# Performance work log

Measured on AMD Instinct MI355X. Metric: run time of the kernel, lower is better.

The kernel has to match this reference:

```python
import jax, jax.numpy as jnp
import numpy as np
from jax import lax


def _batch_conv(x, w, b):
    # x: [B, Cin, H, W], w: [B, Cout, Cin, kh, kw], b: [B, Cout]
    # Per-sample conv (the torch code's groups=B grouped-conv trick),
    # expressed as vmap over the batch of an ordinary conv.
    def one(xi, wi):
        return lax.conv_general_dilated(
            xi[None], wi, window_strides=(1, 1), padding='SAME',
            dimension_numbers=('NCHW', 'OIHW', 'NCHW'))[0]
    y = jax.vmap(one)(x, w)                       # [B, Cout, H, W]
    return y + b[:, :, None, None]


def setup_inputs() -> dict:
    key = jax.random.key(0)
    ks = jax.random.split(key, 9)
    B, Cin, H, W = 32, 3, 64, 64
    NC = 10
    s = 0.05
    return {
        'x': jax.random.normal(ks[0], (B, Cin, H, W), jnp.float32),
        'conv1_weight': jax.random.normal(ks[1], (B, 64, Cin, 3, 3), jnp.float32) * s,
        'conv2_weight': jax.random.normal(ks[2], (B, 128, 64, 3, 3), jnp.float32) * s,
        'conv3_weight': jax.random.normal(ks[3], (B, 256, 128, 3, 3), jnp.float32) * s,
        'fc_weight': jax.random.normal(ks[4], (B, 1, NC), jnp.float32) * s,
        'bias1': jax.random.normal(ks[5], (B, 64), jnp.float32) * s,
        'bias2': jax.random.normal(ks[6], (B, 128), jnp.float32) * s,
        'bias3': jax.random.normal(ks[7], (B, 256), jnp.float32) * s,
        'bias4': jax.random.normal(ks[8], (B, NC), jnp.float32) * s,
    }


def reference(x, conv1_weight, conv2_weight, conv3_weight, fc_weight,
              bias1, bias2, bias3, bias4):
    h = jax.nn.relu(_batch_conv(x, conv1_weight, bias1))   # [B, 64, H, W]
    h = jax.nn.relu(_batch_conv(h, conv2_weight, bias2))   # [B, 128, H, W]
    h = jax.nn.relu(_batch_conv(h, conv3_weight, bias3))   # [B, 256, H, W]
    h = jnp.mean(h, axis=(2, 3))                           # AdaptiveAvgPool2d(1) -> [B, 256]
    h = h[:, :, None]                                      # view(B, N, -1) -> [B, 256, 1]
    # BatchLinearLayer: bmm(x, weight) + bias
    out = jnp.einsum('bnd,bdo->bno', h, fc_weight) + bias4[:, None, :]  # [B, 256, 10]
    return out
```

## Files before the change

kernel.cpp:

```cpp
#include <hip/hip_runtime.h>
#include <stdint.h>

typedef __attribute__((ext_vector_type(8))) short short8;
typedef __attribute__((ext_vector_type(16))) float f32x16;

#define NB 32

__device__ __forceinline__ float bf2f(uint16_t v) {
    return __uint_as_float(((uint32_t)v) << 16);
}
__device__ __forceinline__ uint16_t f2bf(float f) {
    uint32_t u = __float_as_uint(f);
    u += 0x7fffu + ((u >> 16) & 1u);
    return (uint16_t)(u >> 16);
}

__device__ __forceinline__ void gload16(const void* g, void* l) {
    __builtin_amdgcn_global_load_lds(
        (const __attribute__((address_space(1))) uint32_t*)g,
        (__attribute__((address_space(3))) uint32_t*)l, 16, 0, 0);
}

template<int COUT, int CIN>
__device__ __forceinline__ void prep_w_item(int idx, const float* __restrict__ w,
                                            uint16_t* __restrict__ wp)
{
    const int ci = idx % CIN;
    const int t  = idx / CIN;
    const int oc = t % COUT;
    const int b  = t / COUT;
    const float* s = w + (size_t)idx * 9;
    #pragma unroll
    for (int k = 0; k < 9; k++)
        wp[((size_t)(b * 9 + k) * COUT + oc) * CIN + ci] = f2bf(s[k]);
}

__global__ __launch_bounds__(256) void prep_w3_k(
    const float* __restrict__ w, uint16_t* __restrict__ wp)
{
    const int idx = blockIdx.x * 256 + threadIdx.x;
    if (idx < NB * 256 * 128) prep_w_item<256, 128>(idx, w, wp);
}

template<bool DO_W3>
__global__ __launch_bounds__(256) void prep_all(
    const float* __restrict__ x,  const float* __restrict__ w1,
    const float* __restrict__ w2, const float* __restrict__ w3,
    uint16_t* __restrict__ xp,  uint16_t* __restrict__ wp1,
    uint16_t* __restrict__ wp2, uint16_t* __restrict__ wp3,
    float* __restrict__ zp)
{
    int idx = blockIdx.x * 256 + threadIdx.x;
    if (idx < 4096) {
        ((float4*)zp)[idx] = make_float4(0.f, 0.f, 0.f, 0.f);
        return;
    }
    idx -= 4096;
    if (idx < 131072) {
        const int xc = idx & 63, y = (idx >> 6) & 63, b = idx >> 12;
        const float* s = x + (size_t)b * 3 * 4096 + y * 64 + xc;
        const uint16_t v0 = f2bf(s[0]), v1 = f2bf(s[4096]), v2 = f2bf(s[8192]);
        short8 lo = {(short)v0, (short)v1, (short)v2, 0, 0, 0, 0, 0};
        short8 hi = {0, 0, 0, 0, 0, 0, 0, 0};
        uint16_t* d = xp + (size_t)idx * 16;
        *(short8*)d = lo;
        *(short8*)(d + 8) = hi;
        return;
    }
    idx -= 131072;
    if (idx < 18432) {
        const int oc = idx & 63, k = (idx >> 6) % 9, b = idx / 576;
        const uint16_t v0 = f2bf(w1[((size_t)(b * 64 + oc) * 3 + 0) * 9 + k]);
        const uint16_t v1 = f2bf(w1[((size_t)(b * 64 + oc) * 3 + 1) * 9 + k]);
        const uint16_t v2 = f2bf(w1[((size_t)(b * 64 + oc) * 3 + 2) * 9 + k]);
        short8 lo = {(short)v0, (short)v1, (short)v2, 0, 0, 0, 0, 0};
        short8 hi = {0, 0, 0, 0, 0, 0, 0, 0};
        uint16_t* d = wp1 + ((size_t)(b * 9 + k) * 64 + oc) * 16;
        *(short8*)d = lo;
        *(short8*)(d + 8) = hi;
        return;
    }
    idx -= 18432;
    if (idx < 262144) {
        prep_w_item<128, 64>(idx, w2, wp2);
        return;
    }
    if (!DO_W3) return;
    idx -= 262144;
    if (idx < 1048576) prep_w_item<256, 128>(idx, w3, wp3);
}

template<int CIN, int COUT, int OCBLKS, bool POOL>
__global__ __launch_bounds__(256, 2) void conv_mfma(
    const uint16_t* __restrict__ in, const uint16_t* __restrict__ wp,
    const float* __restrict__ bias, uint16_t* __restrict__ out,
    float* __restrict__ partial, const float* __restrict__ zp)
{
    constexpr int IN_CH = 21;
    constexpr int W_CH  = 18;
    constexpr int IN_B  = IN_CH * 1024;
    constexpr int BUF_B = IN_B + W_CH * 1024;
    constexpr int P     = OCBLKS * 8;
    extern __shared__ __align__(16) char sm[];

    const int L   = blockIdx.x;
    const int xcd = L & 7;
    const int jj  = L >> 3;
    const int b   = (jj / P) * 8 + xcd;
    const int inner = jj % P;
    const int ocbase = (inner >> 3) * 64;
    const int stripe = inner & 7;
    const int y0 = stripe * 8;

    const int tid = threadIdx.x;
    const int wv = tid >> 6, l = tid & 63, q = l >> 5, ln = l & 31;
    const int NK = CIN / 16;

    const uint16_t* srcp[10];
    int ldsoff[10];
    #pragma unroll
    for (int j = 0; j < 10; j++) {
        const int chunk = wv * 10 + j;
        if (chunk >= IN_CH + W_CH) {
            srcp[j] = (const uint16_t*)zp;
            ldsoff[j] = -1;
        } else if (chunk < IN_CH) {
            const int gp = chunk * 64 + l;
            const int rq = gp / 66, px = gp - rq * 66;
            const int row = rq >> 1, qq = rq & 1;
            const int gy = y0 - 1 + row, gx = px - 1;
            const bool valid = (rq < 20) && ((unsigned)gy < 64u) && ((unsigned)gx < 64u);
            srcp[j] = valid ? in + ((size_t)((b * 64 + gy) * 64 + gx) * CIN + qq * 8)
                            : (const uint16_t*)zp;
            ldsoff[j] = chunk * 1024;
        } else {
            const int c2 = chunk - IN_CH;
            const int kk = c2 >> 1, qq = c2 & 1, oc = l;
            srcp[j] = wp + ((size_t)(b * 9 + kk) * COUT + ocbase + oc) * CIN + qq * 8;
            ldsoff[j] = IN_B + c2 * 1024;
        }
    }

    int aoffA[4][2];
    #pragma unroll
    for (int t = 0; t < 4; t++)
        #pragma unroll
        for (int h = 0; h < 2; h++)
            aoffA[t][h] = ((((wv * 2 + t) * 2 + q) * 66) + h * 32 + ln) * 16;
    const int boffB = q * 1024 + ln * 16;

    f32x16 aA0, aA1, aB0, aB1, aC0, aC1, aD0, aD1;
    {
        const float bv0 = bias[b * COUT + ocbase + ln];
        const float bv1 = bias[b * COUT + ocbase + 32 + ln];
        #pragma unroll
        for (int r = 0; r < 16; r++) {
            aA0[r] = bv0; aB0[r] = bv0; aC0[r] = bv0; aD0[r] = bv0;
            aA1[r] = bv1; aB1[r] = bv1; aC1[r] = bv1; aD1[r] = bv1;
        }
    }

    auto stage = [&](int bufsel, int k) {
        const int koff = k * 16;
        char* base = sm + bufsel * BUF_B;
        #pragma unroll
        for (int j = 0; j < 10; j++) {
            char* dst = (ldsoff[j] < 0) ? (sm + 2 * BUF_B)
                                        : (base + ldsoff[j]);
            gload16(srcp[j] + koff, dst);
        }
    };

    stage(0, 0);
    if (NK > 1) stage(1, 1);

    for (int k = 0; k < NK; k++) {
        const char* cb = sm + (k & 1) * BUF_B;
        if (k + 1 < NK) asm volatile("s_waitcnt vmcnt(10)" ::: "memory");
        else            asm volatile("s_waitcnt vmcnt(0)"  ::: "memory");
        __builtin_amdgcn_s_barrier();
        __builtin_amdgcn_sched_barrier(0);
        __builtin_amdgcn_s_setprio(1);
        #pragma unroll
        for (int kx = 0; kx < 3; kx++) {
            short8 fA[4][2];
            #pragma unroll
            for (int t = 0; t < 4; t++)
                #pragma unroll
                for (int h = 0; h < 2; h++)
                    fA[t][h] = *(const short8*)(cb + aoffA[t][h] + kx * 16);
            #pragma unroll
            for (int ky = 0; ky < 3; ky++) {
                const int kk = ky * 3 + kx;
                const char* bw = cb + IN_B + kk * 2048 + boffB;
                short8 b0 = *(const short8*)(bw);
                short8 b1 = *(const short8*)(bw + 512);
                aA0 = __builtin_amdgcn_mfma_f32_32x32x16_bf16(fA[ky][0], b0, aA0, 0, 0, 0);
                aB0 = __builtin_amdgcn_mfma_f32_32x32x16_bf16(fA[ky][1], b0, aB0, 0, 0, 0);
                aC0 = __builtin_amdgcn_mfma_f32_32x32x16_bf16(fA[ky + 1][0], b0, aC0, 0, 0, 0);
                aD0 = __builtin_amdgcn_mfma_f32_32x32x16_bf16(fA[ky + 1][1], b0, aD0, 0, 0, 0);
                aA1 = __builtin_amdgcn_mfma_f32_32x32x16_bf16(fA[ky][0], b1, aA1, 0, 0, 0);
                aB1 = __builtin_amdgcn_mfma_f32_32x32x16_bf16(fA[ky][1], b1, aB1, 0, 0, 0);
                aC1 = __builtin_amdgcn_mfma_f32_32x32x16_bf16(fA[ky + 1][0], b1, aC1, 0, 0, 0);
                aD1 = __builtin_amdgcn_mfma_f32_32x32x16_bf16(fA[ky + 1][1], b1, aD1, 0, 0, 0);
            }
        }
        __builtin_amdgcn_s_setprio(0);
        __builtin_amdgcn_s_barrier();
        if (k + 2 < NK) stage(k & 1, k + 2);
    }

    if (!POOL) {
        #pragma unroll
        for (int r = 0; r < 16; r++) {
            const int pxr = (r & 3) + 8 * (r >> 2) + 4 * q;
            const int y0w = y0 + wv * 2;
            uint16_t* dA = out + (size_t)((b * 64 + y0w) * 64 + pxr) * COUT + ocbase;
            uint16_t* dB = out + (size_t)((b * 64 + y0w) * 64 + 32 + pxr) * COUT + ocbase;
            uint16_t* dC = out + (size_t)((b * 64 + y0w + 1) * 64 + pxr) * COUT + ocbase;
            uint16_t* dD = out + (size_t)((b * 64 + y0w + 1) * 64 + 32 + pxr) * COUT + ocbase;
            dA[ln]      = f2bf(fmaxf(aA0[r], 0.f));
            dA[32 + ln] = f2bf(fmaxf(aA1[r], 0.f));
            dB[ln]      = f2bf(fmaxf(aB0[r], 0.f));
            dB[32 + ln] = f2bf(fmaxf(aB1[r], 0.f));
            dC[ln]      = f2bf(fmaxf(aC0[r], 0.f));
            dC[32 + ln] = f2bf(fmaxf(aC1[r], 0.f));
            dD[ln]      = f2bf(fmaxf(aD0[r], 0.f));
            dD[32 + ln] = f2bf(fmaxf(aD1[r], 0.f));
        }
    } else {
        float* red = (float*)(sm + 2 * BUF_B + 1024);
        float s0 = 0.f, s1 = 0.f;
        #pragma unroll
        for (int r = 0; r < 16; r++) {
            s0 += fmaxf(aA0[r], 0.f) + fmaxf(aB0[r], 0.f)
                + fmaxf(aC0[r], 0.f) + fmaxf(aD0[r], 0.f);
            s1 += fmaxf(aA1[r], 0.f) + fmaxf(aB1[r], 0.f)
                + fmaxf(aC1[r], 0.f) + fmaxf(aD1[r], 0.f);
        }
        s0 += __shfl_xor(s0, 32);
        s1 += __shfl_xor(s1, 32);
        if (q == 0) {
            red[wv * 64 + ln] = s0;
            red[wv * 64 + 32 + ln] = s1;
        }
        __syncthreads();
        if (tid < 64) {
            float t = red[tid] + red[64 + tid] + red[128 + tid] + red[192 + tid];
            partial[(size_t)(b * 256 + ocbase + tid) * 8 + stripe] = t;
        }
    }
}

__global__ void fc_k(const float* __restrict__ partial,
                     const float* __restrict__ fcw,
                     const float* __restrict__ b4, float* __restrict__ out)
{
    const int b = blockIdx.x, c = threadIdx.x;
    const float* p = partial + (size_t)(b * 256 + c) * 8;
    float s = 0.f;
    #pragma unroll
    for (int i = 0; i < 8; i++) s += p[i];
    const float pooled = s * (1.f / 4096.f);
    #pragma unroll
    for (int o = 0; o < 10; o++)
        out[(b * 256 + c) * 10 + o] = fmaf(pooled, fcw[b * 10 + o], b4[b * 10 + o]);
}

extern "C" void kernel_launch(void* const* d_in, const int* in_sizes, int n_in,
                              void* d_out, int out_size, void* d_ws, size_t ws_size,
                              hipStream_t stream)
{
    const float* x   = (const float*)d_in[0];
    const float* w1  = (const float*)d_in[1];
    const float* w2  = (const float*)d_in[2];
    const float* w3  = (const float*)d_in[3];
    const float* fcw = (const float*)d_in[4];
    const float* b1  = (const float*)d_in[5];
    const float* b2  = (const float*)d_in[6];
    const float* b3  = (const float*)d_in[7];
    const float* b4  = (const float*)d_in[8];
    char* ws = (char*)d_ws;
    uint16_t* xp  = (uint16_t*)(ws);
    uint16_t* wp1 = (uint16_t*)(ws + 4194304);
    uint16_t* h2  = (uint16_t*)(ws);
    uint16_t* h1  = (uint16_t*)(ws + 33554432);
    uint16_t* wp2 = (uint16_t*)(ws + 50331648);
    const bool big_ws = ws_size >= 74186752u;
    uint16_t* wp3     = (uint16_t*)(ws + (big_ws ? 55050240u : 33554432u));
    float*    partial = (float*)   (ws + (big_ws ? 73924608u : 52428800u));
    float*    zp      = (float*)d_out;

    constexpr int DYN_LDS = 2 * 39936 + 1024 + 1024;
    static bool attr_done = false;
    if (!attr_done) {
        hipFuncSetAttribute((const void*)&conv_mfma<16, 64, 1, false>,
                            hipFuncAttributeMaxDynamicSharedMemorySize, DYN_LDS);
        hipFuncSetAttribute((const void*)&conv_mfma<64, 128, 2, false>,
                            hipFuncAttributeMaxDynamicSharedMemorySize, DYN_LDS);
        hipFuncSetAttribute((const void*)&conv_mfma<128, 256, 4, true>,
                            hipFuncAttributeMaxDynamicSharedMemorySize, DYN_LDS);
        attr_done = true;
    }

    if (big_ws) {
        prep_all<true><<<5720, 256, 0, stream>>>(x, w1, w2, w3, xp, wp1, wp2, wp3, zp);
    } else {
        prep_all<false><<<1624, 256, 0, stream>>>(x, w1, w2, w3, xp, wp1, wp2, wp3, zp);
    }
    conv_mfma<16, 64, 1, false><<<NB * 8, 256, DYN_LDS, stream>>>(xp, wp1, b1, h1, nullptr, zp);
    conv_mfma<64, 128, 2, false><<<NB * 16, 256, DYN_LDS, stream>>>(h1, wp2, b2, h2, nullptr, zp);
    if (!big_ws)
        prep_w3_k<<<4096, 256, 0, stream>>>(w3, wp3);
    conv_mfma<128, 256, 4, true><<<NB * 32, 256, DYN_LDS, stream>>>(h2, wp3, b3, nullptr, partial, zp);
    fc_k<<<NB, 256, 0, stream>>>(partial, fcw, b4, (float*)d_out);
}
```

Baseline: 132.9 us.

## Split conv block work across eight waves to halve per-wave accumulators

Each conv block now runs 512 threads (8 waves) instead of 256. Each wave computes one 32-pixel half of its two rows, so it holds four accumulator tiles instead of eight and issues half the global-to-LDS loads. This cuts register pressure and raises the number of waves available to hide latency. Each A-fragment LDS read now feeds only two MFMAs instead of four, so LDS traffic per MFMA goes up, and barrier cost grows with more waves. The pool reduction gains an extra barrier because its scratch now overlaps the zero-pad area of LDS.

```diff
diff --git a/kernel.cpp b/kernel.cpp
--- a/kernel.cpp
+++ b/kernel.cpp
@@ -91,7 +91,7 @@
 }
 
 template<int CIN, int COUT, int OCBLKS, bool POOL>
-__global__ __launch_bounds__(256, 2) void conv_mfma(
+__global__ __launch_bounds__(512, 4) void conv_mfma(
     const uint16_t* __restrict__ in, const uint16_t* __restrict__ wp,
     const float* __restrict__ bias, uint16_t* __restrict__ out,
     float* __restrict__ partial, const float* __restrict__ zp)
@@ -113,14 +113,16 @@
     const int y0 = stripe * 8;
 
     const int tid = threadIdx.x;
-    const int wv = tid >> 6, l = tid & 63, q = l >> 5, ln = l & 31;
+    const int w  = tid >> 6;
+    const int wv = w >> 1, h = w & 1;
+    const int l  = tid & 63, q = l >> 5, ln = l & 31;
     const int NK = CIN / 16;
 
-    const uint16_t* srcp[10];
-    int ldsoff[10];
-    #pragma unroll
-    for (int j = 0; j < 10; j++) {
-        const int chunk = wv * 10 + j;
+    const uint16_t* srcp[5];
+    int ldsoff[5];
+    #pragma unroll
+    for (int j = 0; j < 5; j++) {
+        const int chunk = w * 5 + j;
         if (chunk >= IN_CH + W_CH) {
             srcp[j] = (const uint16_t*)zp;
             ldsoff[j] = -1;
@@ -141,22 +143,20 @@
         }
     }
 
-    int aoffA[4][2];
+    int aoffA[4];
     #pragma unroll
     for (int t = 0; t < 4; t++)
-        #pragma unroll
-        for (int h = 0; h < 2; h++)
-            aoffA[t][h] = ((((wv * 2 + t) * 2 + q) * 66) + h * 32 + ln) * 16;
+        aoffA[t] = ((((wv * 2 + t) * 2 + q) * 66) + h * 32 + ln) * 16;
     const int boffB = q * 1024 + ln * 16;
 
-    f32x16 aA0, aA1, aB0, aB1, aC0, aC1, aD0, aD1;
+    f32x16 aA0, aA1, aC0, aC1;
     {
         const float bv0 = bias[b * COUT + ocbase + ln];
         const float bv1 = bias[b * COUT + ocbase + 32 + ln];
         #pragma unroll
         for (int r = 0; r < 16; r++) {
-            aA0[r] = bv0; aB0[r] = bv0; aC0[r] = bv0; aD0[r] = bv0;
-            aA1[r] = bv1; aB1[r] = bv1; aC1[r] = bv1; aD1[r] = bv1;
+            aA0[r] = bv0; aC0[r] = bv0;
+            aA1[r] = bv1; aC1[r] = bv1;
         }
     }
 
@@ -164,7 +164,7 @@
         const int koff = k * 16;
         char* base = sm + bufsel * BUF_B;
         #pragma unroll
-        for (int j = 0; j < 10; j++) {
+        for (int j = 0; j < 5; j++) {
             char* dst = (ldsoff[j] < 0) ? (sm + 2 * BUF_B)
                                         : (base + ldsoff[j]);
             gload16(srcp[j] + koff, dst);
@@ -176,33 +176,27 @@
 
     for (int k = 0; k < NK; k++) {
         const char* cb = sm + (k & 1) * BUF_B;
-        if (k + 1 < NK) asm volatile("s_waitcnt vmcnt(10)" ::: "memory");
-        else            asm volatile("s_waitcnt vmcnt(0)"  ::: "memory");
+        if (k + 1 < NK) asm volatile("s_waitcnt vmcnt(5)" ::: "memory");
+        else            asm volatile("s_waitcnt vmcnt(0)" ::: "memory");
         __builtin_amdgcn_s_barrier();
         __builtin_amdgcn_sched_barrier(0);
         __builtin_amdgcn_s_setprio(1);
         #pragma unroll
         for (int kx = 0; kx < 3; kx++) {
-            short8 fA[4][2];
+            short8 fA[4];
             #pragma unroll
             for (int t = 0; t < 4; t++)
-                #pragma unroll
-                for (int h = 0; h < 2; h++)
-                    fA[t][h] = *(const short8*)(cb + aoffA[t][h] + kx * 16);
+                fA[t] = *(const short8*)(cb + aoffA[t] + kx * 16);
             #pragma unroll
             for (int ky = 0; ky < 3; ky++) {
                 const int kk = ky * 3 + kx;
                 const char* bw = cb + IN_B + kk * 2048 + boffB;
                 short8 b0 = *(const short8*)(bw);
                 short8 b1 = *(const short8*)(bw + 512);
-                aA0 = __builtin_amdgcn_mfma_f32_32x32x16_bf16(fA[ky][0], b0, aA0, 0, 0, 0);
-                aB0 = __builtin_amdgcn_mfma_f32_32x32x16_bf16(fA[ky][1], b0, aB0, 0, 0, 0);
-                aC0 = __builtin_amdgcn_mfma_f32_32x32x16_bf16(fA[ky + 1][0], b0, aC0, 0, 0, 0);
-                aD0 = __builtin_amdgcn_mfma_f32_32x32x16_bf16(fA[ky + 1][1], b0, aD0, 0, 0, 0);
-                aA1 = __builtin_amdgcn_mfma_f32_32x32x16_bf16(fA[ky][0], b1, aA1, 0, 0, 0);
-                aB1 = __builtin_amdgcn_mfma_f32_32x32x16_bf16(fA[ky][1], b1, aB1, 0, 0, 0);
-                aC1 = __builtin_amdgcn_mfma_f32_32x32x16_bf16(fA[ky + 1][0], b1, aC1, 0, 0, 0);
-                aD1 = __builtin_amdgcn_mfma_f32_32x32x16_bf16(fA[ky + 1][1], b1, aD1, 0, 0, 0);
+                aA0 = __builtin_amdgcn_mfma_f32_32x32x16_bf16(fA[ky], b0, aA0, 0, 0, 0);
+                aA1 = __builtin_amdgcn_mfma_f32_32x32x16_bf16(fA[ky], b1, aA1, 0, 0, 0);
+                aC0 = __builtin_amdgcn_mfma_f32_32x32x16_bf16(fA[ky + 1], b0, aC0, 0, 0, 0);
+                aC1 = __builtin_amdgcn_mfma_f32_32x32x16_bf16(fA[ky + 1], b1, aC1, 0, 0, 0);
             }
         }
         __builtin_amdgcn_s_setprio(0);
@@ -213,40 +207,35 @@
     if (!POOL) {
         #pragma unroll
         for (int r = 0; r < 16; r++) {
-            const int pxr = (r & 3) + 8 * (r >> 2) + 4 * q;
+            const int pxr = h * 32 + (r & 3) + 8 * (r >> 2) + 4 * q;
             const int y0w = y0 + wv * 2;
             uint16_t* dA = out + (size_t)((b * 64 + y0w) * 64 + pxr) * COUT + ocbase;
-            uint16_t* dB = out + (size_t)((b * 64 + y0w) * 64 + 32 + pxr) * COUT + ocbase;
             uint16_t* dC = out + (size_t)((b * 64 + y0w + 1) * 64 + pxr) * COUT + ocbase;
-            uint16_t* dD = out + (size_t)((b * 64 + y0w + 1) * 64 + 32 + pxr) * COUT + ocbase;
             dA[ln]      = f2bf(fmaxf(aA0[r], 0.f));
             dA[32 + ln] = f2bf(fmaxf(aA1[r], 0.f));
-            dB[ln]      = f2bf(fmaxf(aB0[r], 0.f));
-            dB[32 + ln] = f2bf(fmaxf(aB1[r], 0.f));
             dC[ln]      = f2bf(fmaxf(aC0[r], 0.f));
             dC[32 + ln] = f2bf(fmaxf(aC1[r], 0.f));
-            dD[ln]      = f2bf(fmaxf(aD0[r], 0.f));
-            dD[32 + ln] = f2bf(fmaxf(aD1[r], 0.f));
         }
     } else {
-        float* red = (float*)(sm + 2 * BUF_B + 1024);
+        float* red = (float*)(sm + 2 * BUF_B);
         float s0 = 0.f, s1 = 0.f;
         #pragma unroll
         for (int r = 0; r < 16; r++) {
-            s0 += fmaxf(aA0[r], 0.f) + fmaxf(aB0[r], 0.f)
-                + fmaxf(aC0[r], 0.f) + fmaxf(aD0[r], 0.f);
-            s1 += fmaxf(aA1[r], 0.f) + fmaxf(aB1[r], 0.f)
-                + fmaxf(aC1[r], 0.f) + fmaxf(aD1[r], 0.f);
+            s0 += fmaxf(aA0[r], 0.f) + fmaxf(aC0[r], 0.f);
+            s1 += fmaxf(aA1[r], 0.f) + fmaxf(aC1[r], 0.f);
         }
         s0 += __shfl_xor(s0, 32);
         s1 += __shfl_xor(s1, 32);
+        __syncthreads();
         if (q == 0) {
-            red[wv * 64 + ln] = s0;
-            red[wv * 64 + 32 + ln] = s1;
+            red[w * 64 + ln] = s0;
+            red[w * 64 + 32 + ln] = s1;
         }
         __syncthreads();
         if (tid < 64) {
-            float t = red[tid] + red[64 + tid] + red[128 + tid] + red[192 + tid];
+            float t = 0.f;
+            #pragma unroll
+            for (int i = 0; i < 8; i++) t += red[i * 64 + tid];
             partial[(size_t)(b * 256 + ocbase + tid) * 8 + stripe] = t;
         }
     }
@@ -291,7 +280,7 @@
     float*    partial = (float*)   (ws + (big_ws ? 73924608u : 52428800u));
     float*    zp      = (float*)d_out;
 
-    constexpr int DYN_LDS = 2 * 39936 + 1024 + 1024;
+    constexpr int DYN_LDS = 2 * 39936 + 2048;
     static bool attr_done = false;
     if (!attr_done) {
         hipFuncSetAttribute((const void*)&conv_mfma<16, 64, 1, false>,
@@ -308,10 +297,10 @@
     } else {
         prep_all<false><<<1624, 256, 0, stream>>>(x, w1, w2, w3, xp, wp1, wp2, wp3, zp);
     }
-    conv_mfma<16, 64, 1, false><<<NB * 8, 256, DYN_LDS, stream>>>(xp, wp1, b1, h1, nullptr, zp);
-    conv_mfma<64, 128, 2, false><<<NB * 16, 256, DYN_LDS, stream>>>(h1, wp2, b2, h2, nullptr, zp);
+    conv_mfma<16, 64, 1, false><<<NB * 8, 512, DYN_LDS, stream>>>(xp, wp1, b1, h1, nullptr, zp);
+    conv_mfma<64, 128, 2, false><<<NB * 16, 512, DYN_LDS, stream>>>(h1, wp2, b2, h2, nullptr, zp);
     if (!big_ws)
         prep_w3_k<<<4096, 256, 0, stream>>>(w3, wp3);
-    conv_mfma<128, 256, 4, true><<<NB * 32, 256, DYN_LDS, stream>>>(h2, wp3, b3, nullptr, partial, zp);
+    conv_mfma<128, 256, 4, true><<<NB * 32, 512, DYN_LDS, stream>>>(h2, wp3, b3, nullptr, partial, zp);
     fc_k<<<NB, 256, 0, stream>>>(partial, fcw, b4, (float*)d_out);
 }
```

New measurement: 133.8 us. No clear change (+0.7%).
